# Kernel tuning notes

Measured on AMD Instinct MI355X. Metric: run time of the kernel, lower is better.

The kernel has to match this reference:

```python
import jax, jax.numpy as jnp
import numpy as np

N, E = 50000, 800000
F_IN, F_EMB1, F_EMB2, F_HID, F_OUT = 128, 512, 128, 1024, 64


def _linear_params(k, fan_in, fan_out):
    s = 1.0 / np.sqrt(fan_in)
    kw, kb = jax.random.split(k)
    W = jax.random.uniform(kw, (fan_in, fan_out), jnp.float32, -s, s)
    b = jax.random.uniform(kb, (fan_out,), jnp.float32, -s, s)
    return W, b


def setup_inputs() -> dict:
    key = jax.random.key(0)
    ks = jax.random.split(key, 8)
    x = jax.random.normal(ks[0], (N, F_IN), jnp.float32)
    src = jax.random.randint(ks[1], (E,), 0, N)
    dst = jax.random.randint(ks[2], (E,), 0, N)
    edge_index = jnp.stack([src, dst])  # [2, E]
    edge_weight = jax.random.uniform(ks[3], (E,), jnp.float32)  # positive weights
    W1, b1 = _linear_params(ks[4], F_IN, F_EMB1)
    W2, b2 = _linear_params(ks[5], F_EMB1, F_EMB2)
    W3, b3 = _linear_params(ks[6], F_EMB2, F_HID)
    W4, b4 = _linear_params(ks[7], F_HID, F_OUT)
    return dict(x=x, edge_index=edge_index, edge_weight=edge_weight,
                W1=W1, b1=b1, W2=W2, b2=b2, W3=W3, b3=b3, W4=W4, b4=b4)


def gcn_conv(x, src, dst, w, W, b):
    """PyG GCNConv: transform, then sym-normalized weighted aggregation with self-loops.
    out = D^{-1/2} (A_w + I) D^{-1/2} (x W) + b,  deg = scatter(w @ dst) + 1."""
    n = x.shape[0]
    h = x @ W  # [N, F_out]
    deg = jax.ops.segment_sum(w, dst, num_segments=n) + 1.0  # +1 for self-loop weight
    dinv = jax.lax.rsqrt(deg)
    norm = dinv[src] * w * dinv[dst]  # [E]
    agg = jax.ops.segment_sum(norm[:, None] * h[src], dst, num_segments=n)
    agg = agg + h / deg[:, None]  # self-loop: dinv[i]*1*dinv[i] * h[i]
    return agg + b


def reference(x, edge_index, edge_weight, W1, b1, W2, b2, W3, b3, W4, b4):
    src, dst = edge_index[0], edge_index[1]
    h = jax.nn.relu(gcn_conv(x, src, dst, edge_weight, W1, b1))
    # graph_normalization=False -> identity; dropout is identity in eval mode
    h = jax.nn.relu(gcn_conv(h, src, dst, edge_weight, W2, b2))
    h = jax.nn.relu(h @ W3 + b3)
    out = jax.nn.relu(h @ W4 + b4)
    return out
```

## Files before the change

### kernel.cpp

```cpp
#include <hip/hip_runtime.h>


#define ELLW 64

typedef short bf16x8 __attribute__((ext_vector_type(8)));
typedef float f32x4 __attribute__((ext_vector_type(4)));

__device__ __forceinline__ unsigned short f2b(float f) {
    unsigned u = __builtin_bit_cast(unsigned, f);
    unsigned r = (u + 0x7FFFu + ((u >> 16) & 1u)) >> 16;
    return (unsigned short)r;
}
__device__ __forceinline__ float b2f(unsigned short u) {
    return __builtin_bit_cast(float, (unsigned)u << 16);
}

__global__ void k_setup(const float* __restrict__ x,
                        const float* __restrict__ W1, const float* __restrict__ W2,
                        const float* __restrict__ W3, const float* __restrict__ W4,
                        unsigned short* __restrict__ W1t, unsigned short* __restrict__ W2t,
                        unsigned short* __restrict__ W3t, unsigned short* __restrict__ W4t,
                        unsigned short* __restrict__ xb, int* __restrict__ cnt, int Nn) {
    int b = blockIdx.x;
    if (b < 196) {
        int i = b * 256 + threadIdx.x;
        if (i < Nn) cnt[i] = 0;
    } else if (b < 1476) {
        int i = (b - 196) * 256 + threadIdx.x;
        if (i < 65536) {
            int k = i >> 9, n = i & 511;
            W1t[n * 128 + k] = f2b(W1[i]);
        } else if (i < 131072) {
            int j = i - 65536; int k = j >> 7, n = j & 127;
            W2t[n * 512 + k] = f2b(W2[j]);
        } else if (i < 262144) {
            int j = i - 131072; int k = j >> 10, n = j & 1023;
            W3t[n * 128 + k] = f2b(W3[j]);
        } else {
            int j = i - 262144; int k = j >> 6, n = j & 63;
            W4t[n * 1024 + k] = f2b(W4[j]);
        }
    } else {
        int i = (b - 1476) * 256 + threadIdx.x;
        if (i < Nn * 32) {
            float4 v = ((const float4*)x)[i];
            ushort4 o;
            o.x = f2b(v.x); o.y = f2b(v.y); o.z = f2b(v.z); o.w = f2b(v.w);
            ((ushort4*)xb)[i] = o;
        }
    }
}

__global__ void k_fill_ell(const int* __restrict__ src, const int* __restrict__ dst,
                           const float* __restrict__ w, int* __restrict__ cnt,
                           int2* __restrict__ s_edge, int E) {
    int e = blockIdx.x * 256 + threadIdx.x;
    if (e >= E) return;
    int d = dst[e];
    int2 rec = make_int2(src[e], __builtin_bit_cast(int, w[e]));
    int slot = atomicAdd(&cnt[d], 1);
    if (slot < ELLW) s_edge[(size_t)d * ELLW + slot] = rec;
}

__global__ __launch_bounds__(256) void k_deg(const int2* __restrict__ s_edge,
                                             const int* __restrict__ cnt,
                                             float* __restrict__ dinv, int Nn) {
    int node = blockIdx.x * 4 + (threadIdx.x >> 6);
    if (node >= Nn) return;
    int lane = threadIdx.x & 63;
    int c = min(cnt[node], ELLW);
    float s = 0.0f;
    if (lane < c) s = __builtin_bit_cast(float, s_edge[(size_t)node * ELLW + lane].y);
    #pragma unroll
    for (int d = 32; d > 0; d >>= 1) s += __shfl_down(s, d);
    if (lane == 0) dinv[node] = rsqrtf(1.0f + s);
}

template <bool FIRST, bool BIAS_RELU>
__global__ __launch_bounds__(256) void k_gather(
    const unsigned short* __restrict__ Xb, int2* __restrict__ s_edge,
    const int* __restrict__ cnt, const float* __restrict__ dinv,
    const float* __restrict__ bias, unsigned short* __restrict__ outb, int Nn) {
    int node = blockIdx.x * 4 + (threadIdx.x >> 6);
    if (node >= Nn) return;
    int lane = threadIdx.x & 63;
    float di = dinv[node];
    float dii = di * di;
    ushort2 sv = ((const ushort2*)(Xb + (size_t)node * 128))[lane];
    float ax = b2f(sv.x) * dii, ay = b2f(sv.y) * dii;

    int c = min(cnt[node], ELLW);
    size_t base = (size_t)node * ELLW;
    int sreg = 0;
    float nv = 0.0f;
    if (lane < c) {
        int2 rec = s_edge[base + lane];
        sreg = rec.x;
        if (FIRST) {
            float wv = __builtin_bit_cast(float, rec.y);
            nv = dinv[sreg] * wv * di;
            ((int*)s_edge)[2 * (base + lane) + 1] = __builtin_bit_cast(int, nv);
        } else {
            nv = __builtin_bit_cast(float, rec.y);
        }
    }

    int j = 0;
    for (; j + 8 <= c; j += 8) {
        int s0 = __shfl(sreg, j),     s1 = __shfl(sreg, j + 1);
        int s2 = __shfl(sreg, j + 2), s3 = __shfl(sreg, j + 3);
        int s4 = __shfl(sreg, j + 4), s5 = __shfl(sreg, j + 5);
        int s6 = __shfl(sreg, j + 6), s7 = __shfl(sreg, j + 7);
        float n0 = __shfl(nv, j),     n1 = __shfl(nv, j + 1);
        float n2 = __shfl(nv, j + 2), n3 = __shfl(nv, j + 3);
        float n4 = __shfl(nv, j + 4), n5 = __shfl(nv, j + 5);
        float n6 = __shfl(nv, j + 6), n7 = __shfl(nv, j + 7);
        ushort2 r0 = ((const ushort2*)(Xb + (size_t)s0 * 128))[lane];
        ushort2 r1 = ((const ushort2*)(Xb + (size_t)s1 * 128))[lane];
        ushort2 r2 = ((const ushort2*)(Xb + (size_t)s2 * 128))[lane];
        ushort2 r3 = ((const ushort2*)(Xb + (size_t)s3 * 128))[lane];
        ushort2 r4 = ((const ushort2*)(Xb + (size_t)s4 * 128))[lane];
        ushort2 r5 = ((const ushort2*)(Xb + (size_t)s5 * 128))[lane];
        ushort2 r6 = ((const ushort2*)(Xb + (size_t)s6 * 128))[lane];
        ushort2 r7 = ((const ushort2*)(Xb + (size_t)s7 * 128))[lane];
        ax += n0 * b2f(r0.x) + n1 * b2f(r1.x) + n2 * b2f(r2.x) + n3 * b2f(r3.x);
        ay += n0 * b2f(r0.y) + n1 * b2f(r1.y) + n2 * b2f(r2.y) + n3 * b2f(r3.y);
        ax += n4 * b2f(r4.x) + n5 * b2f(r5.x) + n6 * b2f(r6.x) + n7 * b2f(r7.x);
        ay += n4 * b2f(r4.y) + n5 * b2f(r5.y) + n6 * b2f(r6.y) + n7 * b2f(r7.y);
    }
    for (; j < c; ++j) {
        int sj = __shfl(sreg, j);
        float nj = __shfl(nv, j);
        ushort2 r = ((const ushort2*)(Xb + (size_t)sj * 128))[lane];
        ax += nj * b2f(r.x);
        ay += nj * b2f(r.y);
    }

    if (BIAS_RELU) {
        float2 bv = ((const float2*)bias)[lane];
        ax = fmaxf(ax + bv.x, 0.0f);
        ay = fmaxf(ay + bv.y, 0.0f);
    }
    ushort2 o; o.x = f2b(ax); o.y = f2b(ay);
    ((ushort2*)(outb + (size_t)node * 128))[lane] = o;
}

template <int H, int OUTW, bool HAS_BO, bool OUT_BF16>
__global__ __launch_bounds__(256) void k_mlp(
    const unsigned short* __restrict__ A, const unsigned short* __restrict__ Wht,
    const unsigned short* __restrict__ Wot, const float* __restrict__ bh,
    const float* __restrict__ bo, void* __restrict__ out, int M) {
    constexpr int HC = H / 64;
    constexpr int NJ = OUTW / 16;
    constexpr int OW4 = OUTW / 32;
    __shared__ __align__(16) unsigned short Whs[64 * 128];
    __shared__ __align__(16) unsigned short Ps[64 * 64];
    __shared__ __align__(16) unsigned short Wos[OUTW * 64];
    const int tid = threadIdx.x, wave = tid >> 6, lane = tid & 63;
    const int lm = lane & 15, quad = lane >> 4;
    const int bm0 = blockIdx.x * 64;

    bf16x8 af[4];
    {
        int gr = bm0 + wave * 16 + lm;
        #pragma unroll
        for (int kb = 0; kb < 4; ++kb) af[kb] = bf16x8{0, 0, 0, 0, 0, 0, 0, 0};
        if (gr < M) {
            #pragma unroll
            for (int kb = 0; kb < 4; ++kb)
                af[kb] = *(const bf16x8*)(A + (size_t)gr * 128 + kb * 32 + quad * 8);
        }
    }

    #pragma unroll
    for (int u = 0; u < 4; ++u) {
        int idx = tid + u * 256; int r = idx >> 4, g = idx & 15;
        *(int4*)&Whs[r * 128 + ((g ^ (r & 15)) * 8)] =
            *(const int4*)(Wht + (size_t)r * 128 + g * 8);
    }
    #pragma unroll
    for (int u = 0; u < OW4; ++u) {
        int idx = tid + u * 256; int r = idx >> 3, g = idx & 7;
        *(int4*)&Wos[r * 64 + ((g ^ (r & 7)) * 8)] =
            *(const int4*)(Wot + (size_t)r * H + g * 8);
    }
    __syncthreads();

    f32x4 oacc[NJ] = {};
    for (int c = 0; c < HC; ++c) {
        f32x4 hacc[4] = {};
        #pragma unroll
        for (int kb = 0; kb < 4; ++kb) {
            bf16x8 bfr[4];
            #pragma unroll
            for (int j = 0; j < 4; ++j) {
                int r = j * 16 + lm, g = kb * 4 + quad;
                bfr[j] = *(const bf16x8*)&Whs[r * 128 + ((g ^ (r & 15)) * 8)];
            }
            #pragma unroll
            for (int j = 0; j < 4; ++j)
                hacc[j] = __builtin_amdgcn_mfma_f32_16x16x32_bf16(af[kb], bfr[j], hacc[j], 0, 0, 0);
        }

        #pragma unroll
        for (int j = 0; j < 4; ++j) {
            int col = j * 16 + lm;
            float bv = bh[c * 64 + col];
            #pragma unroll
            for (int r4 = 0; r4 < 4; ++r4) {
                int row = wave * 16 + quad * 4 + r4;
                float o = fmaxf(hacc[j][r4] + bv, 0.0f);
                Ps[row * 64 + (((col >> 3) ^ (row & 7)) * 8) + (col & 7)] = f2b(o);
            }
        }

        #pragma unroll
        for (int kb = 0; kb < 2; ++kb) {
            bf16x8 pf;
            {
                int r = wave * 16 + lm, g = kb * 4 + quad;
                pf = *(const bf16x8*)&Ps[r * 64 + ((g ^ (r & 7)) * 8)];
            }
            #pragma unroll
            for (int j = 0; j < NJ; ++j) {
                int r = j * 16 + lm, g = kb * 4 + quad;
                bf16x8 wf = *(const bf16x8*)&Wos[r * 64 + ((g ^ (r & 7)) * 8)];
                oacc[j] = __builtin_amdgcn_mfma_f32_16x16x32_bf16(pf, wf, oacc[j], 0, 0, 0);
            }
        }

        if (c + 1 < HC) {
            __syncthreads();
            #pragma unroll
            for (int u = 0; u < 4; ++u) {
                int idx = tid + u * 256; int r = idx >> 4, g = idx & 15;
                *(int4*)&Whs[r * 128 + ((g ^ (r & 15)) * 8)] =
                    *(const int4*)(Wht + (size_t)((c + 1) * 64 + r) * 128 + g * 8);
            }
            #pragma unroll
            for (int u = 0; u < OW4; ++u) {
                int idx = tid + u * 256; int r = idx >> 3, g = idx & 7;
                *(int4*)&Wos[r * 64 + ((g ^ (r & 7)) * 8)] =
                    *(const int4*)(Wot + (size_t)r * H + (c + 1) * 64 + g * 8);
            }
            __syncthreads();
        }
    }

    #pragma unroll
    for (int j = 0; j < NJ; ++j) {
        int col = j * 16 + lm;
        float bv = HAS_BO ? bo[col] : 0.0f;
        #pragma unroll
        for (int r4 = 0; r4 < 4; ++r4) {
            int m = bm0 + wave * 16 + quad * 4 + r4;
            if (m < M) {
                float o = oacc[j][r4];
                if (HAS_BO) o = fmaxf(o + bv, 0.0f);
                if (OUT_BF16)
                    ((unsigned short*)out)[(size_t)m * OUTW + col] = f2b(o);
                else
                    ((float*)out)[(size_t)m * OUTW + col] = o;
            }
        }
    }
}

static inline int cdiv(long a, long b) { return (int)((a + b - 1) / b); }

extern "C" void kernel_launch(void* const* d_in, const int* in_sizes, int n_in,
                              void* d_out, int out_size, void* d_ws, size_t ws_size,
                              hipStream_t stream) {
    const float* x  = (const float*)d_in[0];
    const int*   ei = (const int*)d_in[1];
    const float* ew = (const float*)d_in[2];
    const float* W1 = (const float*)d_in[3];
    const float* b1 = (const float*)d_in[4];
    const float* W2 = (const float*)d_in[5];
    const float* b2 = (const float*)d_in[6];
    const float* W3 = (const float*)d_in[7];
    const float* b3 = (const float*)d_in[8];
    const float* W4 = (const float*)d_in[9];
    const float* b4 = (const float*)d_in[10];
    const int Nn = in_sizes[0] / 128;
    const int E  = in_sizes[1] / 2;
    const int* src = ei;
    const int* dst = ei + E;

    char* ws = (char*)d_ws;
    size_t off_b = 0;
    auto alloc = [&](size_t bytes) -> void* {
        void* p = ws + off_b;
        off_b += (bytes + 255) & ~(size_t)255;
        return p;
    };
    float*          dinv   = (float*)alloc((size_t)Nn * 4);
    int*            cnt    = (int*)alloc((size_t)Nn * 4);
    int2*           s_edge = (int2*)alloc((size_t)Nn * ELLW * 8);
    unsigned short* W1t    = (unsigned short*)alloc(512 * 128 * 2);
    unsigned short* W2t    = (unsigned short*)alloc(128 * 512 * 2);
    unsigned short* W3t    = (unsigned short*)alloc(1024 * 128 * 2);
    unsigned short* W4t    = (unsigned short*)alloc(64 * 1024 * 2);
    unsigned short* xb     = (unsigned short*)alloc((size_t)Nn * 128 * 2);
    unsigned short* t2b    = (unsigned short*)alloc((size_t)Nn * 128 * 2);
    unsigned short* actb   = (unsigned short*)alloc((size_t)Nn * 128 * 2);
    float*          out    = (float*)d_out;

    k_setup<<<7726, 256, 0, stream>>>(x, W1, W2, W3, W4, W1t, W2t, W3t, W4t, xb, cnt, Nn);
    k_fill_ell<<<cdiv(E, 256), 256, 0, stream>>>(src, dst, ew, cnt, s_edge, E);
    k_deg<<<cdiv(Nn, 4), 256, 0, stream>>>(s_edge, cnt, dinv, Nn);

    k_gather<true, false><<<cdiv(Nn, 4), 256, 0, stream>>>(
        xb, s_edge, cnt, dinv, nullptr, actb, Nn);
    k_mlp<512, 128, false, true><<<cdiv(Nn, 64), 256, 0, stream>>>(
        actb, W1t, W2t, b1, nullptr, t2b, Nn);

    k_gather<false, true><<<cdiv(Nn, 4), 256, 0, stream>>>(
        t2b, s_edge, cnt, dinv, b2, actb, Nn);

    k_mlp<1024, 64, true, false><<<cdiv(Nn, 64), 256, 0, stream>>>(
        actb, W3t, W4t, b3, b4, out, Nn);
}
```

Before: 306.4 us.

## Fuse ELL fill into setup kernel and double MLP row tile, reading Wo directly

The edge-to-ELL fill moves into the setup kernel. Counter zeroing becomes a hipMemsetAsync so the atomics and ELL writes can run alongside the weight and x conversion, saving one launch. The fused MLP now handles 128 rows per block (two 16-row subtiles per wave), so each weight fragment is reused twice and the block count halves. The second-layer weights are no longer staged in shared memory; each wave loads them straight from global/L2. That saves LDS and barrier work but adds uncoalesced global loads inside the inner loop and raises register pressure.

```diff
diff --git a/kernel.cpp b/kernel.cpp
--- a/kernel.cpp
+++ b/kernel.cpp
@@ -20,13 +20,21 @@
                         const float* __restrict__ W3, const float* __restrict__ W4,
                         unsigned short* __restrict__ W1t, unsigned short* __restrict__ W2t,
                         unsigned short* __restrict__ W3t, unsigned short* __restrict__ W4t,
-                        unsigned short* __restrict__ xb, int* __restrict__ cnt, int Nn) {
+                        unsigned short* __restrict__ xb,
+                        const int* __restrict__ src, const int* __restrict__ dst,
+                        const float* __restrict__ ew, int* __restrict__ cnt,
+                        int2* __restrict__ s_edge, int Nn, int E) {
     int b = blockIdx.x;
-    if (b < 196) {
-        int i = b * 256 + threadIdx.x;
-        if (i < Nn) cnt[i] = 0;
-    } else if (b < 1476) {
-        int i = (b - 196) * 256 + threadIdx.x;
+    if (b < 3125) {
+        int e = b * 256 + threadIdx.x;
+        if (e < E) {
+            int d = dst[e];
+            int2 rec = make_int2(src[e], __builtin_bit_cast(int, ew[e]));
+            int slot = atomicAdd(&cnt[d], 1);
+            if (slot < ELLW) s_edge[(size_t)d * ELLW + slot] = rec;
+        }
+    } else if (b < 4405) {
+        int i = (b - 3125) * 256 + threadIdx.x;
         if (i < 65536) {
             int k = i >> 9, n = i & 511;
             W1t[n * 128 + k] = f2b(W1[i]);
@@ -41,7 +49,7 @@
             W4t[n * 1024 + k] = f2b(W4[j]);
         }
     } else {
-        int i = (b - 1476) * 256 + threadIdx.x;
+        int i = (b - 4405) * 256 + threadIdx.x;
         if (i < Nn * 32) {
             float4 v = ((const float4*)x)[i];
             ushort4 o;
@@ -49,17 +57,6 @@
             ((ushort4*)xb)[i] = o;
         }
     }
-}
-
-__global__ void k_fill_ell(const int* __restrict__ src, const int* __restrict__ dst,
-                           const float* __restrict__ w, int* __restrict__ cnt,
-                           int2* __restrict__ s_edge, int E) {
-    int e = blockIdx.x * 256 + threadIdx.x;
-    if (e >= E) return;
-    int d = dst[e];
-    int2 rec = make_int2(src[e], __builtin_bit_cast(int, w[e]));
-    int slot = atomicAdd(&cnt[d], 1);
-    if (slot < ELLW) s_edge[(size_t)d * ELLW + slot] = rec;
 }
 
 __global__ __launch_bounds__(256) void k_deg(const int2* __restrict__ s_edge,
@@ -152,23 +149,22 @@
     const float* __restrict__ bo, void* __restrict__ out, int M) {
     constexpr int HC = H / 64;
     constexpr int NJ = OUTW / 16;
-    constexpr int OW4 = OUTW / 32;
     __shared__ __align__(16) unsigned short Whs[64 * 128];
-    __shared__ __align__(16) unsigned short Ps[64 * 64];
-    __shared__ __align__(16) unsigned short Wos[OUTW * 64];
+    __shared__ __align__(16) unsigned short Ps[128 * 64];
     const int tid = threadIdx.x, wave = tid >> 6, lane = tid & 63;
     const int lm = lane & 15, quad = lane >> 4;
-    const int bm0 = blockIdx.x * 64;
-
-    bf16x8 af[4];
-    {
-        int gr = bm0 + wave * 16 + lm;
-        #pragma unroll
-        for (int kb = 0; kb < 4; ++kb) af[kb] = bf16x8{0, 0, 0, 0, 0, 0, 0, 0};
+    const int bm0 = blockIdx.x * 128;
+
+    bf16x8 af[2][4];
+    #pragma unroll
+    for (int i = 0; i < 2; ++i) {
+        int gr = bm0 + wave * 32 + i * 16 + lm;
+        #pragma unroll
+        for (int kb = 0; kb < 4; ++kb) af[i][kb] = bf16x8{0, 0, 0, 0, 0, 0, 0, 0};
         if (gr < M) {
             #pragma unroll
             for (int kb = 0; kb < 4; ++kb)
-                af[kb] = *(const bf16x8*)(A + (size_t)gr * 128 + kb * 32 + quad * 8);
+                af[i][kb] = *(const bf16x8*)(A + (size_t)gr * 128 + kb * 32 + quad * 8);
         }
     }
 
@@ -178,17 +174,11 @@
         *(int4*)&Whs[r * 128 + ((g ^ (r & 15)) * 8)] =
             *(const int4*)(Wht + (size_t)r * 128 + g * 8);
     }
-    #pragma unroll
-    for (int u = 0; u < OW4; ++u) {
-        int idx = tid + u * 256; int r = idx >> 3, g = idx & 7;
-        *(int4*)&Wos[r * 64 + ((g ^ (r & 7)) * 8)] =
-            *(const int4*)(Wot + (size_t)r * H + g * 8);
-    }
     __syncthreads();
 
-    f32x4 oacc[NJ] = {};
+    f32x4 oacc[2][NJ] = {};
     for (int c = 0; c < HC; ++c) {
-        f32x4 hacc[4] = {};
+        f32x4 hacc[2][4] = {};
         #pragma unroll
         for (int kb = 0; kb < 4; ++kb) {
             bf16x8 bfr[4];
@@ -198,34 +188,44 @@
                 bfr[j] = *(const bf16x8*)&Whs[r * 128 + ((g ^ (r & 15)) * 8)];
             }
             #pragma unroll
-            for (int j = 0; j < 4; ++j)
-                hacc[j] = __builtin_amdgcn_mfma_f32_16x16x32_bf16(af[kb], bfr[j], hacc[j], 0, 0, 0);
-        }
-
-        #pragma unroll
-        for (int j = 0; j < 4; ++j) {
-            int col = j * 16 + lm;
-            float bv = bh[c * 64 + col];
-            #pragma unroll
-            for (int r4 = 0; r4 < 4; ++r4) {
-                int row = wave * 16 + quad * 4 + r4;
-                float o = fmaxf(hacc[j][r4] + bv, 0.0f);
-                Ps[row * 64 + (((col >> 3) ^ (row & 7)) * 8) + (col & 7)] = f2b(o);
+            for (int i = 0; i < 2; ++i)
+                #pragma unroll
+                for (int j = 0; j < 4; ++j)
+                    hacc[i][j] = __builtin_amdgcn_mfma_f32_16x16x32_bf16(
+                        af[i][kb], bfr[j], hacc[i][j], 0, 0, 0);
+        }
+
+        #pragma unroll
+        for (int i = 0; i < 2; ++i) {
+            #pragma unroll
+            for (int j = 0; j < 4; ++j) {
+                int col = j * 16 + lm;
+                float bv = bh[c * 64 + col];
+                #pragma unroll
+                for (int r4 = 0; r4 < 4; ++r4) {
+                    int row = wave * 32 + i * 16 + quad * 4 + r4;
+                    float o = fmaxf(hacc[i][j][r4] + bv, 0.0f);
+                    Ps[row * 64 + (((col >> 3) ^ (row & 7)) * 8) + (col & 7)] = f2b(o);
+                }
             }
         }
 
         #pragma unroll
         for (int kb = 0; kb < 2; ++kb) {
-            bf16x8 pf;
-            {
-                int r = wave * 16 + lm, g = kb * 4 + quad;
-                pf = *(const bf16x8*)&Ps[r * 64 + ((g ^ (r & 7)) * 8)];
+            bf16x8 pf[2];
+            #pragma unroll
+            for (int i = 0; i < 2; ++i) {
+                int r = wave * 32 + i * 16 + lm, g = kb * 4 + quad;
+                pf[i] = *(const bf16x8*)&Ps[r * 64 + ((g ^ (r & 7)) * 8)];
             }
             #pragma unroll
             for (int j = 0; j < NJ; ++j) {
-                int r = j * 16 + lm, g = kb * 4 + quad;
-                bf16x8 wf = *(const bf16x8*)&Wos[r * 64 + ((g ^ (r & 7)) * 8)];
-                oacc[j] = __builtin_amdgcn_mfma_f32_16x16x32_bf16(pf, wf, oacc[j], 0, 0, 0);
+                bf16x8 wf = *(const bf16x8*)(Wot + (size_t)(j * 16 + lm) * H +
+                                             c * 64 + kb * 32 + quad * 8);
+                #pragma unroll
+                for (int i = 0; i < 2; ++i)
+                    oacc[i][j] = __builtin_amdgcn_mfma_f32_16x16x32_bf16(
+                        pf[i], wf, oacc[i][j], 0, 0, 0);
             }
         }
 
@@ -237,30 +237,27 @@
                 *(int4*)&Whs[r * 128 + ((g ^ (r & 15)) * 8)] =
                     *(const int4*)(Wht + (size_t)((c + 1) * 64 + r) * 128 + g * 8);
             }
-            #pragma unroll
-            for (int u = 0; u < OW4; ++u) {
-                int idx = tid + u * 256; int r = idx >> 3, g = idx & 7;
-                *(int4*)&Wos[r * 64 + ((g ^ (r & 7)) * 8)] =
-                    *(const int4*)(Wot + (size_t)r * H + (c + 1) * 64 + g * 8);
-            }
             __syncthreads();
         }
     }
 
     #pragma unroll
-    for (int j = 0; j < NJ; ++j) {
-        int col = j * 16 + lm;
-        float bv = HAS_BO ? bo[col] : 0.0f;
-        #pragma unroll
-        for (int r4 = 0; r4 < 4; ++r4) {
-            int m = bm0 + wave * 16 + quad * 4 + r4;
-            if (m < M) {
-                float o = oacc[j][r4];
-                if (HAS_BO) o = fmaxf(o + bv, 0.0f);
-                if (OUT_BF16)
-                    ((unsigned short*)out)[(size_t)m * OUTW + col] = f2b(o);
-                else
-                    ((float*)out)[(size_t)m * OUTW + col] = o;
+    for (int i = 0; i < 2; ++i) {
+        #pragma unroll
+        for (int j = 0; j < NJ; ++j) {
+            int col = j * 16 + lm;
+            float bv = HAS_BO ? bo[col] : 0.0f;
+            #pragma unroll
+            for (int r4 = 0; r4 < 4; ++r4) {
+                int m = bm0 + wave * 32 + i * 16 + quad * 4 + r4;
+                if (m < M) {
+                    float o = oacc[i][j][r4];
+                    if (HAS_BO) o = fmaxf(o + bv, 0.0f);
+                    if (OUT_BF16)
+                        ((unsigned short*)out)[(size_t)m * OUTW + col] = f2b(o);
+                    else
+                        ((float*)out)[(size_t)m * OUTW + col] = o;
+                }
             }
         }
     }
@@ -306,18 +303,19 @@
     unsigned short* actb   = (unsigned short*)alloc((size_t)Nn * 128 * 2);
     float*          out    = (float*)d_out;
 
-    k_setup<<<7726, 256, 0, stream>>>(x, W1, W2, W3, W4, W1t, W2t, W3t, W4t, xb, cnt, Nn);
-    k_fill_ell<<<cdiv(E, 256), 256, 0, stream>>>(src, dst, ew, cnt, s_edge, E);
+    hipMemsetAsync(cnt, 0, (size_t)Nn * 4, stream);
+    k_setup<<<10655, 256, 0, stream>>>(x, W1, W2, W3, W4, W1t, W2t, W3t, W4t,
+                                       xb, src, dst, ew, cnt, s_edge, Nn, E);
     k_deg<<<cdiv(Nn, 4), 256, 0, stream>>>(s_edge, cnt, dinv, Nn);
 
     k_gather<true, false><<<cdiv(Nn, 4), 256, 0, stream>>>(
         xb, s_edge, cnt, dinv, nullptr, actb, Nn);
-    k_mlp<512, 128, false, true><<<cdiv(Nn, 64), 256, 0, stream>>>(
+    k_mlp<512, 128, false, true><<<cdiv(Nn, 128), 256, 0, stream>>>(
         actb, W1t, W2t, b1, nullptr, t2b, Nn);
 
     k_gather<false, true><<<cdiv(Nn, 4), 256, 0, stream>>>(
         t2b, s_edge, cnt, dinv, b2, actb, Nn);
 
-    k_mlp<1024, 64, true, false><<<cdiv(Nn, 64), 256, 0, stream>>>(
+    k_mlp<1024, 64, true, false><<<cdiv(Nn, 128), 256, 0, stream>>>(
         actb, W3t, W4t, b3, b4, out, Nn);
 }
```

Result: slower. 323.1 us (+5.4%).

## Fuse neighbor gather aggregation into MLP kernels via shared-memory staging

Applied to the files above, without the earlier changes.

Merges each gather kernel with the following two-layer MLP kernel. Each block first aggregates its 64 nodes (16 per wave, sequentially) into a swizzled shared-memory tile, loads the MFMA A fragments from it, then reuses that buffer for the weight tiles. This removes the intermediate activation buffer write and read and two kernel launches. In exchange, the gather runs with fewer, larger blocks and serial per-wave node loops, so fewer memory requests are in flight to hide latency.

```diff
diff --git a/kernel.cpp b/kernel.cpp
--- a/kernel.cpp
+++ b/kernel.cpp
@@ -76,106 +76,106 @@
     if (lane == 0) dinv[node] = rsqrtf(1.0f + s);
 }
 
-template <bool FIRST, bool BIAS_RELU>
-__global__ __launch_bounds__(256) void k_gather(
+template <int H, int OUTW, bool FIRST, bool AGG_BIAS, bool HAS_BO, bool OUT_BF16>
+__global__ __launch_bounds__(256) void k_gmlp(
     const unsigned short* __restrict__ Xb, int2* __restrict__ s_edge,
     const int* __restrict__ cnt, const float* __restrict__ dinv,
-    const float* __restrict__ bias, unsigned short* __restrict__ outb, int Nn) {
-    int node = blockIdx.x * 4 + (threadIdx.x >> 6);
-    if (node >= Nn) return;
-    int lane = threadIdx.x & 63;
-    float di = dinv[node];
-    float dii = di * di;
-    ushort2 sv = ((const ushort2*)(Xb + (size_t)node * 128))[lane];
-    float ax = b2f(sv.x) * dii, ay = b2f(sv.y) * dii;
-
-    int c = min(cnt[node], ELLW);
-    size_t base = (size_t)node * ELLW;
-    int sreg = 0;
-    float nv = 0.0f;
-    if (lane < c) {
-        int2 rec = s_edge[base + lane];
-        sreg = rec.x;
-        if (FIRST) {
-            float wv = __builtin_bit_cast(float, rec.y);
-            nv = dinv[sreg] * wv * di;
-            ((int*)s_edge)[2 * (base + lane) + 1] = __builtin_bit_cast(int, nv);
-        } else {
-            nv = __builtin_bit_cast(float, rec.y);
-        }
-    }
-
-    int j = 0;
-    for (; j + 8 <= c; j += 8) {
-        int s0 = __shfl(sreg, j),     s1 = __shfl(sreg, j + 1);
-        int s2 = __shfl(sreg, j + 2), s3 = __shfl(sreg, j + 3);
-        int s4 = __shfl(sreg, j + 4), s5 = __shfl(sreg, j + 5);
-        int s6 = __shfl(sreg, j + 6), s7 = __shfl(sreg, j + 7);
-        float n0 = __shfl(nv, j),     n1 = __shfl(nv, j + 1);
-        float n2 = __shfl(nv, j + 2), n3 = __shfl(nv, j + 3);
-        float n4 = __shfl(nv, j + 4), n5 = __shfl(nv, j + 5);
-        float n6 = __shfl(nv, j + 6), n7 = __shfl(nv, j + 7);
-        ushort2 r0 = ((const ushort2*)(Xb + (size_t)s0 * 128))[lane];
-        ushort2 r1 = ((const ushort2*)(Xb + (size_t)s1 * 128))[lane];
-        ushort2 r2 = ((const ushort2*)(Xb + (size_t)s2 * 128))[lane];
-        ushort2 r3 = ((const ushort2*)(Xb + (size_t)s3 * 128))[lane];
-        ushort2 r4 = ((const ushort2*)(Xb + (size_t)s4 * 128))[lane];
-        ushort2 r5 = ((const ushort2*)(Xb + (size_t)s5 * 128))[lane];
-        ushort2 r6 = ((const ushort2*)(Xb + (size_t)s6 * 128))[lane];
-        ushort2 r7 = ((const ushort2*)(Xb + (size_t)s7 * 128))[lane];
-        ax += n0 * b2f(r0.x) + n1 * b2f(r1.x) + n2 * b2f(r2.x) + n3 * b2f(r3.x);
-        ay += n0 * b2f(r0.y) + n1 * b2f(r1.y) + n2 * b2f(r2.y) + n3 * b2f(r3.y);
-        ax += n4 * b2f(r4.x) + n5 * b2f(r5.x) + n6 * b2f(r6.x) + n7 * b2f(r7.x);
-        ay += n4 * b2f(r4.y) + n5 * b2f(r5.y) + n6 * b2f(r6.y) + n7 * b2f(r7.y);
-    }
-    for (; j < c; ++j) {
-        int sj = __shfl(sreg, j);
-        float nj = __shfl(nv, j);
-        ushort2 r = ((const ushort2*)(Xb + (size_t)sj * 128))[lane];
-        ax += nj * b2f(r.x);
-        ay += nj * b2f(r.y);
-    }
-
-    if (BIAS_RELU) {
-        float2 bv = ((const float2*)bias)[lane];
-        ax = fmaxf(ax + bv.x, 0.0f);
-        ay = fmaxf(ay + bv.y, 0.0f);
-    }
-    ushort2 o; o.x = f2b(ax); o.y = f2b(ay);
-    ((ushort2*)(outb + (size_t)node * 128))[lane] = o;
-}
-
-template <int H, int OUTW, bool HAS_BO, bool OUT_BF16>
-__global__ __launch_bounds__(256) void k_mlp(
-    const unsigned short* __restrict__ A, const unsigned short* __restrict__ Wht,
-    const unsigned short* __restrict__ Wot, const float* __restrict__ bh,
-    const float* __restrict__ bo, void* __restrict__ out, int M) {
+    const float* __restrict__ agg_bias,
+    const unsigned short* __restrict__ Wht, const unsigned short* __restrict__ Wot,
+    const float* __restrict__ bh, const float* __restrict__ bo,
+    void* __restrict__ out, int Nn) {
     constexpr int HC = H / 64;
     constexpr int NJ = OUTW / 16;
     constexpr int OW4 = OUTW / 32;
-    __shared__ __align__(16) unsigned short Whs[64 * 128];
+    __shared__ __align__(16) unsigned short AWhs[64 * 128];
     __shared__ __align__(16) unsigned short Ps[64 * 64];
     __shared__ __align__(16) unsigned short Wos[OUTW * 64];
     const int tid = threadIdx.x, wave = tid >> 6, lane = tid & 63;
     const int lm = lane & 15, quad = lane >> 4;
     const int bm0 = blockIdx.x * 64;
 
+    for (int t = 0; t < 16; ++t) {
+        int row = wave * 16 + t;
+        int node = bm0 + row;
+        float ax = 0.0f, ay = 0.0f;
+        if (node < Nn) {
+            float di = dinv[node];
+            float dii = di * di;
+            ushort2 sv = ((const ushort2*)(Xb + (size_t)node * 128))[lane];
+            ax = b2f(sv.x) * dii; ay = b2f(sv.y) * dii;
+
+            int c = min(cnt[node], ELLW);
+            size_t base = (size_t)node * ELLW;
+            int sreg = 0;
+            float nv = 0.0f;
+            if (lane < c) {
+                int2 rec = s_edge[base + lane];
+                sreg = rec.x;
+                if (FIRST) {
+                    float wv = __builtin_bit_cast(float, rec.y);
+                    nv = dinv[sreg] * wv * di;
+                    ((int*)s_edge)[2 * (base + lane) + 1] = __builtin_bit_cast(int, nv);
+                } else {
+                    nv = __builtin_bit_cast(float, rec.y);
+                }
+            }
+            int j = 0;
+            for (; j + 8 <= c; j += 8) {
+                int s0 = __shfl(sreg, j),     s1 = __shfl(sreg, j + 1);
+                int s2 = __shfl(sreg, j + 2), s3 = __shfl(sreg, j + 3);
+                int s4 = __shfl(sreg, j + 4), s5 = __shfl(sreg, j + 5);
+                int s6 = __shfl(sreg, j + 6), s7 = __shfl(sreg, j + 7);
+                float n0 = __shfl(nv, j),     n1 = __shfl(nv, j + 1);
+                float n2 = __shfl(nv, j + 2), n3 = __shfl(nv, j + 3);
+                float n4 = __shfl(nv, j + 4), n5 = __shfl(nv, j + 5);
+                float n6 = __shfl(nv, j + 6), n7 = __shfl(nv, j + 7);
+                ushort2 r0 = ((const ushort2*)(Xb + (size_t)s0 * 128))[lane];
+                ushort2 r1 = ((const ushort2*)(Xb + (size_t)s1 * 128))[lane];
+                ushort2 r2 = ((const ushort2*)(Xb + (size_t)s2 * 128))[lane];
+                ushort2 r3 = ((const ushort2*)(Xb + (size_t)s3 * 128))[lane];
+                ushort2 r4 = ((const ushort2*)(Xb + (size_t)s4 * 128))[lane];
+                ushort2 r5 = ((const ushort2*)(Xb + (size_t)s5 * 128))[lane];
+                ushort2 r6 = ((const ushort2*)(Xb + (size_t)s6 * 128))[lane];
+                ushort2 r7 = ((const ushort2*)(Xb + (size_t)s7 * 128))[lane];
+                ax += n0 * b2f(r0.x) + n1 * b2f(r1.x) + n2 * b2f(r2.x) + n3 * b2f(r3.x);
+                ay += n0 * b2f(r0.y) + n1 * b2f(r1.y) + n2 * b2f(r2.y) + n3 * b2f(r3.y);
+                ax += n4 * b2f(r4.x) + n5 * b2f(r5.x) + n6 * b2f(r6.x) + n7 * b2f(r7.x);
+                ay += n4 * b2f(r4.y) + n5 * b2f(r5.y) + n6 * b2f(r6.y) + n7 * b2f(r7.y);
+            }
+            for (; j < c; ++j) {
+                int sj = __shfl(sreg, j);
+                float nj = __shfl(nv, j);
+                ushort2 r = ((const ushort2*)(Xb + (size_t)sj * 128))[lane];
+                ax += nj * b2f(r.x);
+                ay += nj * b2f(r.y);
+            }
+            if (AGG_BIAS) {
+                float2 bv = ((const float2*)agg_bias)[lane];
+                ax = fmaxf(ax + bv.x, 0.0f);
+                ay = fmaxf(ay + bv.y, 0.0f);
+            }
+        }
+        int col = 2 * lane;
+        int g = col >> 3;
+        ushort2 o; o.x = f2b(ax); o.y = f2b(ay);
+        *(ushort2*)&AWhs[row * 128 + ((g ^ (row & 15)) * 8) + (col & 7)] = o;
+    }
+
     bf16x8 af[4];
     {
-        int gr = bm0 + wave * 16 + lm;
-        #pragma unroll
-        for (int kb = 0; kb < 4; ++kb) af[kb] = bf16x8{0, 0, 0, 0, 0, 0, 0, 0};
-        if (gr < M) {
-            #pragma unroll
-            for (int kb = 0; kb < 4; ++kb)
-                af[kb] = *(const bf16x8*)(A + (size_t)gr * 128 + kb * 32 + quad * 8);
-        }
-    }
+        int r = wave * 16 + lm;
+        #pragma unroll
+        for (int kb = 0; kb < 4; ++kb) {
+            int g = kb * 4 + quad;
+            af[kb] = *(const bf16x8*)&AWhs[r * 128 + ((g ^ (r & 15)) * 8)];
+        }
+    }
+    __syncthreads();
 
     #pragma unroll
     for (int u = 0; u < 4; ++u) {
         int idx = tid + u * 256; int r = idx >> 4, g = idx & 15;
-        *(int4*)&Whs[r * 128 + ((g ^ (r & 15)) * 8)] =
+        *(int4*)&AWhs[r * 128 + ((g ^ (r & 15)) * 8)] =
             *(const int4*)(Wht + (size_t)r * 128 + g * 8);
     }
     #pragma unroll
@@ -195,7 +195,7 @@
             #pragma unroll
             for (int j = 0; j < 4; ++j) {
                 int r = j * 16 + lm, g = kb * 4 + quad;
-                bfr[j] = *(const bf16x8*)&Whs[r * 128 + ((g ^ (r & 15)) * 8)];
+                bfr[j] = *(const bf16x8*)&AWhs[r * 128 + ((g ^ (r & 15)) * 8)];
             }
             #pragma unroll
             for (int j = 0; j < 4; ++j)
@@ -234,7 +234,7 @@
             #pragma unroll
             for (int u = 0; u < 4; ++u) {
                 int idx = tid + u * 256; int r = idx >> 4, g = idx & 15;
-                *(int4*)&Whs[r * 128 + ((g ^ (r & 15)) * 8)] =
+                *(int4*)&AWhs[r * 128 + ((g ^ (r & 15)) * 8)] =
                     *(const int4*)(Wht + (size_t)((c + 1) * 64 + r) * 128 + g * 8);
             }
             #pragma unroll
@@ -254,7 +254,7 @@
         #pragma unroll
         for (int r4 = 0; r4 < 4; ++r4) {
             int m = bm0 + wave * 16 + quad * 4 + r4;
-            if (m < M) {
+            if (m < Nn) {
                 float o = oacc[j][r4];
                 if (HAS_BO) o = fmaxf(o + bv, 0.0f);
                 if (OUT_BF16)
@@ -303,21 +303,15 @@
     unsigned short* W4t    = (unsigned short*)alloc(64 * 1024 * 2);
     unsigned short* xb     = (unsigned short*)alloc((size_t)Nn * 128 * 2);
     unsigned short* t2b    = (unsigned short*)alloc((size_t)Nn * 128 * 2);
-    unsigned short* actb   = (unsigned short*)alloc((size_t)Nn * 128 * 2);
     float*          out    = (float*)d_out;
 
     k_setup<<<7726, 256, 0, stream>>>(x, W1, W2, W3, W4, W1t, W2t, W3t, W4t, xb, cnt, Nn);
     k_fill_ell<<<cdiv(E, 256), 256, 0, stream>>>(src, dst, ew, cnt, s_edge, E);
     k_deg<<<cdiv(Nn, 4), 256, 0, stream>>>(s_edge, cnt, dinv, Nn);
 
-    k_gather<true, false><<<cdiv(Nn, 4), 256, 0, stream>>>(
-        xb, s_edge, cnt, dinv, nullptr, actb, Nn);
-    k_mlp<512, 128, false, true><<<cdiv(Nn, 64), 256, 0, stream>>>(
-        actb, W1t, W2t, b1, nullptr, t2b, Nn);
-
-    k_gather<false, true><<<cdiv(Nn, 4), 256, 0, stream>>>(
-        t2b, s_edge, cnt, dinv, b2, actb, Nn);
-
-    k_mlp<1024, 64, true, false><<<cdiv(Nn, 64), 256, 0, stream>>>(
-        actb, W3t, W4t, b3, b4, out, Nn);
-}
+    k_gmlp<512, 128, true, false, false, true><<<cdiv(Nn, 64), 256, 0, stream>>>(
+        xb, s_edge, cnt, dinv, nullptr, W1t, W2t, b1, nullptr, t2b, Nn);
+
+    k_gmlp<1024, 64, false, true, true, false><<<cdiv(Nn, 64), 256, 0, stream>>>(
+        t2b, s_edge, cnt, dinv, b2, W3t, W4t, b3, b4, out, Nn);
+}
```

Result: slower. 380.0 us (+24.0%).

## Merge ELL fill into setup kernel and read MLP output weights from global

Applied to the files above, without the earlier changes.

The edge-to-ELL fill is folded into the setup kernel as extra blocks, with the counter reset done by an async memset instead, so one launch goes away. In the fused MLP kernel the second-layer weight tile is no longer staged in shared memory; each wave reads its weight fragments straight from global/L2. This cuts LDS use and the per-chunk copy work, but adds uncoalesced global loads inside the inner MFMA loop.

```diff
diff --git a/kernel.cpp b/kernel.cpp
--- a/kernel.cpp
+++ b/kernel.cpp
@@ -20,13 +20,21 @@
                         const float* __restrict__ W3, const float* __restrict__ W4,
                         unsigned short* __restrict__ W1t, unsigned short* __restrict__ W2t,
                         unsigned short* __restrict__ W3t, unsigned short* __restrict__ W4t,
-                        unsigned short* __restrict__ xb, int* __restrict__ cnt, int Nn) {
+                        unsigned short* __restrict__ xb,
+                        const int* __restrict__ src, const int* __restrict__ dst,
+                        const float* __restrict__ ew, int* __restrict__ cnt,
+                        int2* __restrict__ s_edge, int Nn, int E) {
     int b = blockIdx.x;
-    if (b < 196) {
-        int i = b * 256 + threadIdx.x;
-        if (i < Nn) cnt[i] = 0;
-    } else if (b < 1476) {
-        int i = (b - 196) * 256 + threadIdx.x;
+    if (b < 3125) {
+        int e = b * 256 + threadIdx.x;
+        if (e < E) {
+            int d = dst[e];
+            int2 rec = make_int2(src[e], __builtin_bit_cast(int, ew[e]));
+            int slot = atomicAdd(&cnt[d], 1);
+            if (slot < ELLW) s_edge[(size_t)d * ELLW + slot] = rec;
+        }
+    } else if (b < 4405) {
+        int i = (b - 3125) * 256 + threadIdx.x;
         if (i < 65536) {
             int k = i >> 9, n = i & 511;
             W1t[n * 128 + k] = f2b(W1[i]);
@@ -41,7 +49,7 @@
             W4t[n * 1024 + k] = f2b(W4[j]);
         }
     } else {
-        int i = (b - 1476) * 256 + threadIdx.x;
+        int i = (b - 4405) * 256 + threadIdx.x;
         if (i < Nn * 32) {
             float4 v = ((const float4*)x)[i];
             ushort4 o;
@@ -49,17 +57,6 @@
             ((ushort4*)xb)[i] = o;
         }
     }
-}
-
-__global__ void k_fill_ell(const int* __restrict__ src, const int* __restrict__ dst,
-                           const float* __restrict__ w, int* __restrict__ cnt,
-                           int2* __restrict__ s_edge, int E) {
-    int e = blockIdx.x * 256 + threadIdx.x;
-    if (e >= E) return;
-    int d = dst[e];
-    int2 rec = make_int2(src[e], __builtin_bit_cast(int, w[e]));
-    int slot = atomicAdd(&cnt[d], 1);
-    if (slot < ELLW) s_edge[(size_t)d * ELLW + slot] = rec;
 }
 
 __global__ __launch_bounds__(256) void k_deg(const int2* __restrict__ s_edge,
@@ -152,10 +149,8 @@
     const float* __restrict__ bo, void* __restrict__ out, int M) {
     constexpr int HC = H / 64;
     constexpr int NJ = OUTW / 16;
-    constexpr int OW4 = OUTW / 32;
     __shared__ __align__(16) unsigned short Whs[64 * 128];
     __shared__ __align__(16) unsigned short Ps[64 * 64];
-    __shared__ __align__(16) unsigned short Wos[OUTW * 64];
     const int tid = threadIdx.x, wave = tid >> 6, lane = tid & 63;
     const int lm = lane & 15, quad = lane >> 4;
     const int bm0 = blockIdx.x * 64;
@@ -178,12 +173,6 @@
         *(int4*)&Whs[r * 128 + ((g ^ (r & 15)) * 8)] =
             *(const int4*)(Wht + (size_t)r * 128 + g * 8);
     }
-    #pragma unroll
-    for (int u = 0; u < OW4; ++u) {
-        int idx = tid + u * 256; int r = idx >> 3, g = idx & 7;
-        *(int4*)&Wos[r * 64 + ((g ^ (r & 7)) * 8)] =
-            *(const int4*)(Wot + (size_t)r * H + g * 8);
-    }
     __syncthreads();
 
     f32x4 oacc[NJ] = {};
@@ -223,8 +212,8 @@
             }
             #pragma unroll
             for (int j = 0; j < NJ; ++j) {
-                int r = j * 16 + lm, g = kb * 4 + quad;
-                bf16x8 wf = *(const bf16x8*)&Wos[r * 64 + ((g ^ (r & 7)) * 8)];
+                bf16x8 wf = *(const bf16x8*)(Wot + (size_t)(j * 16 + lm) * H +
+                                             c * 64 + kb * 32 + quad * 8);
                 oacc[j] = __builtin_amdgcn_mfma_f32_16x16x32_bf16(pf, wf, oacc[j], 0, 0, 0);
             }
         }
@@ -236,12 +225,6 @@
                 int idx = tid + u * 256; int r = idx >> 4, g = idx & 15;
                 *(int4*)&Whs[r * 128 + ((g ^ (r & 15)) * 8)] =
                     *(const int4*)(Wht + (size_t)((c + 1) * 64 + r) * 128 + g * 8);
-            }
-            #pragma unroll
-            for (int u = 0; u < OW4; ++u) {
-                int idx = tid + u * 256; int r = idx >> 3, g = idx & 7;
-                *(int4*)&Wos[r * 64 + ((g ^ (r & 7)) * 8)] =
-                    *(const int4*)(Wot + (size_t)r * H + (c + 1) * 64 + g * 8);
             }
             __syncthreads();
         }
@@ -306,8 +289,9 @@
     unsigned short* actb   = (unsigned short*)alloc((size_t)Nn * 128 * 2);
     float*          out    = (float*)d_out;
 
-    k_setup<<<7726, 256, 0, stream>>>(x, W1, W2, W3, W4, W1t, W2t, W3t, W4t, xb, cnt, Nn);
-    k_fill_ell<<<cdiv(E, 256), 256, 0, stream>>>(src, dst, ew, cnt, s_edge, E);
+    hipMemsetAsync(cnt, 0, (size_t)Nn * 4, stream);
+    k_setup<<<10655, 256, 0, stream>>>(x, W1, W2, W3, W4, W1t, W2t, W3t, W4t,
+                                       xb, src, dst, ew, cnt, s_edge, Nn, E);
     k_deg<<<cdiv(Nn, 4), 256, 0, stream>>>(s_edge, cnt, dinv, Nn);
 
     k_gather<true, false><<<cdiv(Nn, 4), 256, 0, stream>>>(
```

Result: slower. 358.2 us (+16.9%).
